# Kernel optimization log

Hardware: AMD Instinct MI355X
Metric: run time of the kernel (lower is better)

Reference implementation:

```python
import jax, jax.numpy as jnp
import numpy as np


def setup_inputs() -> dict:
    key = jax.random.key(0)
    k1, k2 = jax.random.split(key)
    B, S, D = 32, 2048, 1024
    decoder_hidden = jax.random.normal(k1, (1, B, D), dtype=jnp.float32)
    encoder_outputs = jax.random.normal(k2, (S, B, D), dtype=jnp.float32)
    return {"decoder_hidden": decoder_hidden, "encoder_outputs": encoder_outputs}


def reference(decoder_hidden, encoder_outputs):
    # decoder_hidden: (1, B, D); encoder_outputs: (S, B, D)
    query = decoder_hidden[0]                      # (B, D)
    kv = jnp.transpose(encoder_outputs, (1, 0, 2)) # (B, S, D)
    energy = jnp.einsum('bsd,bd->bs', kv, query)   # dot-product scores (B, S)
    attn_scores = jax.nn.softmax(energy, axis=-1)  # (B, S)
    attn_values = jnp.einsum('bsd,bs->bd', kv, attn_scores)  # (B, D)
    return (attn_values, attn_scores)
```

## Files before the change

kernel.cpp:

```cpp
#include <hip/hip_runtime.h>
#include <math.h>

#define BB 32
#define SS 2048
#define DD 1024


template <int NCH>
__global__ __launch_bounds__(256, 8) void fused_pass(const float* __restrict__ q,
                                                     const float* __restrict__ enc,
                                                     float* __restrict__ energy,
                                                     float* __restrict__ partial,
                                                     float* __restrict__ ml) {
    constexpr int CHS = SS / NCH;
    int blk = blockIdx.x;
    int b   = blk / NCH;
    int cb  = blk % NCH;
    int tid = threadIdx.x;
    int wid = tid >> 6;
    int ln  = tid & 63;

    __shared__ float red[2][4];

    float4 qv = ((const float4*)(q + (size_t)b * DD))[tid];

    int s0 = cb * CHS;
    const float4* base = (const float4*)enc;
    const size_t rs = (size_t)BB * (DD / 4);
    size_t idx = (size_t)(s0 * BB + b) * (DD / 4) + tid;

    float m = -1e30f, l = 0.f;
    float4 acc = {0.f, 0.f, 0.f, 0.f};
    float4 v = base[idx];

    for (int i = 0; i < CHS; ++i) {
        float4 vn = {0.f, 0.f, 0.f, 0.f};
        if (i + 1 < CHS) vn = base[idx + (size_t)(i + 1) * rs];

        float pd = v.x * qv.x + v.y * qv.y + v.z * qv.z + v.w * qv.w;
#pragma unroll
        for (int off = 32; off > 0; off >>= 1)
            pd += __shfl_xor(pd, off, 64);
        if (ln == 0) red[i & 1][wid] = pd;
        __syncthreads();
        float e = red[i & 1][0] + red[i & 1][1] + red[i & 1][2] + red[i & 1][3];

        if (tid == 0) energy[b * SS + s0 + i] = e;

        float mn    = fmaxf(m, e);
        float scale = __expf(m - mn);
        float p     = __expf(e - mn);
        l = l * scale + p;
        acc.x = acc.x * scale + p * v.x;
        acc.y = acc.y * scale + p * v.y;
        acc.z = acc.z * scale + p * v.z;
        acc.w = acc.w * scale + p * v.w;
        m = mn;
        v = vn;
    }

    ((float4*)(partial + (size_t)blk * DD))[tid] = acc;
    if (tid == 0) { ml[blk * 2] = m; ml[blk * 2 + 1] = l; }
}

__global__ __launch_bounds__(256) void merge_scores(const float* __restrict__ partial,
                                                    const float* __restrict__ ml,
                                                    const float* __restrict__ energy,
                                                    float* __restrict__ values,
                                                    float* __restrict__ scores,
                                                    int nch) {
    int blk  = blockIdx.x;
    int b    = blk >> 2;
    int quad = blk & 3;
    int tid  = threadIdx.x;
    __shared__ float sm[64], sl[64];

    if (tid < nch) {
        sm[tid] = ml[(b * nch + tid) * 2];
        sl[tid] = ml[(b * nch + tid) * 2 + 1];
    }
    __syncthreads();

    float M = -1e30f;
    for (int c = 0; c < nch; ++c) M = fmaxf(M, sm[c]);

    int d = quad * 256 + tid;
    float L = 0.f, acc = 0.f;
    for (int c = 0; c < nch; ++c) {
        float w = __expf(sm[c] - M);
        L += w * sl[c];
        acc += w * partial[(size_t)(b * nch + c) * DD + d];
    }
    float inv = 1.f / L;
    values[b * DD + d] = acc * inv;

#pragma unroll
    for (int k = 0; k < 2; ++k) {
        int idx = b * SS + quad * 512 + k * 256 + tid;
        scores[idx] = __expf(energy[idx] - M) * inv;
    }
}

extern "C" void kernel_launch(void* const* d_in, const int* in_sizes, int n_in,
                              void* d_out, int out_size, void* d_ws, size_t ws_size,
                              hipStream_t stream) {
    const float* q   = (const float*)d_in[0];
    const float* enc = (const float*)d_in[1];
    float* out    = (float*)d_out;
    float* values = out;
    float* scores = out + BB * DD;

    size_t need64 = ((size_t)BB * SS + (size_t)BB * 64 * DD + (size_t)BB * 64 * 2)
                    * sizeof(float);
    int nch = (ws_size >= need64) ? 64 : 32;

    float* energy  = (float*)d_ws;
    float* partial = energy + BB * SS;
    float* ml      = partial + (size_t)BB * nch * DD;

    if (nch == 64)
        fused_pass<64><<<BB * 64, 256, 0, stream>>>(q, enc, energy, partial, ml);
    else
        fused_pass<32><<<BB * 32, 256, 0, stream>>>(q, enc, energy, partial, ml);
    merge_scores<<<BB * 4, 256, 0, stream>>>(partial, ml, energy, values, scores, nch);
}
```

Before: 55.00 us.

## Process four rows per iteration with batched reductions and lazy softmax rescale

The fused pass now loads and prefetches four encoder rows at a time. It computes four dot products, reduces them through shared memory with one wave per row, and updates the online softmax once per group. Rescaling is skipped unless the running max grows by more than 8, which cuts exp calls and barrier count per row while using more registers (launch bounds drop to 4 blocks). The merge kernel now runs 8 blocks per batch and precomputes the chunk weights once in shared memory.

```diff
diff --git a/kernel.cpp b/kernel.cpp
--- a/kernel.cpp
+++ b/kernel.cpp
@@ -7,12 +7,13 @@
 
 
 template <int NCH>
-__global__ __launch_bounds__(256, 8) void fused_pass(const float* __restrict__ q,
+__global__ __launch_bounds__(256, 4) void fused_pass(const float* __restrict__ q,
                                                      const float* __restrict__ enc,
                                                      float* __restrict__ energy,
                                                      float* __restrict__ partial,
                                                      float* __restrict__ ml) {
     constexpr int CHS = SS / NCH;
+    constexpr int NR  = CHS / 4;
     int blk = blockIdx.x;
     int b   = blk / NCH;
     int cb  = blk % NCH;
@@ -20,7 +21,8 @@
     int wid = tid >> 6;
     int ln  = tid & 63;
 
-    __shared__ float red[2][4];
+    __shared__ float pdl[4][256];
+    __shared__ float ew[4];
 
     float4 qv = ((const float4*)(q + (size_t)b * DD))[tid];
 
@@ -31,32 +33,60 @@
 
     float m = -1e30f, l = 0.f;
     float4 acc = {0.f, 0.f, 0.f, 0.f};
-    float4 v = base[idx];
+    float4 vc[4], vn[4];
 
-    for (int i = 0; i < CHS; ++i) {
-        float4 vn = {0.f, 0.f, 0.f, 0.f};
-        if (i + 1 < CHS) vn = base[idx + (size_t)(i + 1) * rs];
+#pragma unroll
+    for (int j = 0; j < 4; ++j) vc[j] = base[idx + (size_t)j * rs];
 
-        float pd = v.x * qv.x + v.y * qv.y + v.z * qv.z + v.w * qv.w;
+#pragma unroll 2
+    for (int r = 0; r < NR; ++r) {
+        if (r + 1 < NR) {
 #pragma unroll
-        for (int off = 32; off > 0; off >>= 1)
-            pd += __shfl_xor(pd, off, 64);
-        if (ln == 0) red[i & 1][wid] = pd;
+            for (int j = 0; j < 4; ++j)
+                vn[j] = base[idx + (size_t)((r + 1) * 4 + j) * rs];
+        }
+
+        float pd[4];
+#pragma unroll
+        for (int j = 0; j < 4; ++j) {
+            float4 v = vc[j];
+            pd[j] = v.x * qv.x + v.y * qv.y + v.z * qv.z + v.w * qv.w;
+        }
+#pragma unroll
+        for (int j = 0; j < 4; ++j) pdl[j][tid] = pd[j];
         __syncthreads();
-        float e = red[i & 1][0] + red[i & 1][1] + red[i & 1][2] + red[i & 1][3];
 
-        if (tid == 0) energy[b * SS + s0 + i] = e;
+        {
+            float4 t = ((const float4*)pdl[wid])[ln];
+            float s = t.x + t.y + t.z + t.w;
+#pragma unroll
+            for (int off = 32; off > 0; off >>= 1)
+                s += __shfl_xor(s, off, 64);
+            if (ln == 0) {
+                ew[wid] = s;
+                energy[b * SS + s0 + r * 4 + wid] = s;
+            }
+        }
+        __syncthreads();
 
-        float mn    = fmaxf(m, e);
-        float scale = __expf(m - mn);
-        float p     = __expf(e - mn);
-        l = l * scale + p;
-        acc.x = acc.x * scale + p * v.x;
-        acc.y = acc.y * scale + p * v.y;
-        acc.z = acc.z * scale + p * v.z;
-        acc.w = acc.w * scale + p * v.w;
-        m = mn;
-        v = vn;
+        float e0 = ew[0], e1 = ew[1], e2 = ew[2], e3 = ew[3];
+        float pmax = fmaxf(fmaxf(e0, e1), fmaxf(e2, e3));
+        if (pmax > m + 8.f) {
+            float sc = __expf(m - pmax);
+            l *= sc;
+            acc.x *= sc; acc.y *= sc; acc.z *= sc; acc.w *= sc;
+            m = pmax;
+        }
+        float p0 = __expf(e0 - m), p1 = __expf(e1 - m);
+        float p2 = __expf(e2 - m), p3 = __expf(e3 - m);
+        l += p0 + p1 + p2 + p3;
+        acc.x += p0 * vc[0].x + p1 * vc[1].x + p2 * vc[2].x + p3 * vc[3].x;
+        acc.y += p0 * vc[0].y + p1 * vc[1].y + p2 * vc[2].y + p3 * vc[3].y;
+        acc.z += p0 * vc[0].z + p1 * vc[1].z + p2 * vc[2].z + p3 * vc[3].z;
+        acc.w += p0 * vc[0].w + p1 * vc[1].w + p2 * vc[2].w + p3 * vc[3].w;
+
+#pragma unroll
+        for (int j = 0; j < 4; ++j) vc[j] = vn[j];
     }
 
     ((float4*)(partial + (size_t)blk * DD))[tid] = acc;
@@ -69,11 +99,11 @@
                                                     float* __restrict__ values,
                                                     float* __restrict__ scores,
                                                     int nch) {
-    int blk  = blockIdx.x;
-    int b    = blk >> 2;
-    int quad = blk & 3;
-    int tid  = threadIdx.x;
-    __shared__ float sm[64], sl[64];
+    int blk = blockIdx.x;
+    int b   = blk >> 3;
+    int oct = blk & 7;
+    int tid = threadIdx.x;
+    __shared__ float sm[64], sl[64], sw[64];
 
     if (tid < nch) {
         sm[tid] = ml[(b * nch + tid) * 2];
@@ -83,22 +113,23 @@
 
     float M = -1e30f;
     for (int c = 0; c < nch; ++c) M = fmaxf(M, sm[c]);
+    if (tid < nch) sw[tid] = __expf(sm[tid] - M);
+    __syncthreads();
 
-    int d = quad * 256 + tid;
-    float L = 0.f, acc = 0.f;
-    for (int c = 0; c < nch; ++c) {
-        float w = __expf(sm[c] - M);
-        L += w * sl[c];
-        acc += w * partial[(size_t)(b * nch + c) * DD + d];
+    float L = 0.f;
+    for (int c = 0; c < nch; ++c) L += sw[c] * sl[c];
+    float inv = 1.f / L;
+
+    if (tid < 128) {
+        int d = oct * 128 + tid;
+        float acc = 0.f;
+        for (int c = 0; c < nch; ++c)
+            acc += sw[c] * partial[(size_t)(b * nch + c) * DD + d];
+        values[b * DD + d] = acc * inv;
     }
-    float inv = 1.f / L;
-    values[b * DD + d] = acc * inv;
 
-#pragma unroll
-    for (int k = 0; k < 2; ++k) {
-        int idx = b * SS + quad * 512 + k * 256 + tid;
-        scores[idx] = __expf(energy[idx] - M) * inv;
-    }
+    int sidx = b * SS + oct * 256 + tid;
+    scores[sidx] = __expf(energy[sidx] - M) * inv;
 }
 
 extern "C" void kernel_launch(void* const* d_in, const int* in_sizes, int n_in,
@@ -122,5 +153,5 @@
         fused_pass<64><<<BB * 64, 256, 0, stream>>>(q, enc, energy, partial, ml);
     else
         fused_pass<32><<<BB * 32, 256, 0, stream>>>(q, enc, energy, partial, ml);
-    merge_scores<<<BB * 4, 256, 0, stream>>>(partial, ml, energy, values, scores, nch);
+    merge_scores<<<BB * 8, 256, 0, stream>>>(partial, ml, energy, values, scores, nch);
 }
```

New measurement: 56.71 us. 3.1% more time.
